# Optimization experiments

Measured on AMD Instinct MI355X. Metric: run time of the kernel, lower is better.

The kernel has to match this reference:

```python
import jax, jax.numpy as jnp
import numpy as np

N = 50000          # nodes
E = 800000         # edges (before self loops)
C_IN, HID, C_OUT, L = 128, 64, 64, 3
LSTM_H = (L * HID) // 2   # 96, PyG JK-LSTM hidden size
NEG_SLOPE = 0.2


def gat_conv(x, src, dst, W, a_src, a_dst, b):
    # single-head PyG GATConv
    h = x @ W.T                                  # [N, HID]
    al = h @ a_src                               # [N] src attention logits
    ar = h @ a_dst                               # [N]
    e = jax.nn.leaky_relu(al[src] + ar[dst], NEG_SLOPE)   # [E+N]
    m = jax.ops.segment_max(e, dst, num_segments=N)
    ex = jnp.exp(e - m[dst])
    den = jax.ops.segment_sum(ex, dst, num_segments=N)
    coef = ex / den[dst]                         # segment softmax over dst neighborhoods
    out = jax.ops.segment_sum(coef[:, None] * h[src], dst, num_segments=N)
    return out + b


def lstm_dir(seq, Wih, Whh, bih, bhh, reverse):
    # seq: [L, N, C]; returns hidden states [L, N, H] in original time order
    H = Whh.shape[1]
    h0 = jnp.zeros((seq.shape[1], H), seq.dtype)

    def step(carry, x_t):
        h, c = carry
        g = x_t @ Wih.T + bih + h @ Whh.T + bhh
        i, f, gg, o = jnp.split(g, 4, axis=-1)
        c = jax.nn.sigmoid(f) * c + jax.nn.sigmoid(i) * jnp.tanh(gg)
        h = jax.nn.sigmoid(o) * jnp.tanh(c)
        return (h, c), h

    _, hs = jax.lax.scan(step, (h0, h0), seq, reverse=reverse)
    return hs


def setup_inputs() -> dict:
    key = jax.random.key(0)
    ks = jax.random.split(key, 32)
    s = 0.1
    inp = {
        'x': jax.random.normal(ks[0], (N, C_IN), jnp.float32),
        'edge_index': jax.random.randint(ks[1], (2, E), 0, N, jnp.int64
                                         if jax.config.jax_enable_x64 else jnp.int32),
    }
    dims = [C_IN, HID, HID]
    for l in range(L):
        inp[f'conv{l}_W'] = s * jax.random.normal(ks[2 + 4 * l], (HID, dims[l]), jnp.float32)
        inp[f'conv{l}_asrc'] = s * jax.random.normal(ks[3 + 4 * l], (HID,), jnp.float32)
        inp[f'conv{l}_adst'] = s * jax.random.normal(ks[4 + 4 * l], (HID,), jnp.float32)
        inp[f'conv{l}_b'] = jnp.zeros((HID,), jnp.float32)
    for d, off in (('f', 16), ('b', 20)):
        inp[f'lstm_Wih_{d}'] = s * jax.random.normal(ks[off], (4 * LSTM_H, HID), jnp.float32)
        inp[f'lstm_Whh_{d}'] = s * jax.random.normal(ks[off + 1], (4 * LSTM_H, LSTM_H), jnp.float32)
        inp[f'lstm_bih_{d}'] = jnp.zeros((4 * LSTM_H,), jnp.float32)
        inp[f'lstm_bhh_{d}'] = jnp.zeros((4 * LSTM_H,), jnp.float32)
    inp['att_W'] = s * jax.random.normal(ks[24], (1, 2 * LSTM_H), jnp.float32)
    inp['att_b'] = jnp.zeros((1,), jnp.float32)
    inp['out_W'] = s * jax.random.normal(ks[25], (C_OUT, HID), jnp.float32)
    inp['out_b'] = jnp.zeros((C_OUT,), jnp.float32)
    return inp


def reference(x, edge_index,
              conv0_W, conv0_asrc, conv0_adst, conv0_b,
              conv1_W, conv1_asrc, conv1_adst, conv1_b,
              conv2_W, conv2_asrc, conv2_adst, conv2_b,
              lstm_Wih_f, lstm_Whh_f, lstm_bih_f, lstm_bhh_f,
              lstm_Wih_b, lstm_Whh_b, lstm_bih_b, lstm_bhh_b,
              att_W, att_b, out_W, out_b):
    # add self loops (PyG GATConv default)
    loop = jnp.arange(N, dtype=edge_index.dtype)
    src = jnp.concatenate([edge_index[0], loop])
    dst = jnp.concatenate([edge_index[1], loop])

    convs = [(conv0_W, conv0_asrc, conv0_adst, conv0_b),
             (conv1_W, conv1_asrc, conv1_adst, conv1_b),
             (conv2_W, conv2_asrc, conv2_adst, conv2_b)]
    xs = []
    h = x
    for (W, asrc, adst, b) in convs:
        h = jax.nn.relu(gat_conv(h, src, dst, W, asrc, adst, b))
        xs.append(h)

    seq = jnp.stack(xs, axis=0)                       # [L, N, HID]
    hf = lstm_dir(seq, lstm_Wih_f, lstm_Whh_f, lstm_bih_f, lstm_bhh_f, False)
    hb = lstm_dir(seq, lstm_Wih_b, lstm_Whh_b, lstm_bih_b, lstm_bhh_b, True)
    hcat = jnp.concatenate([hf, hb], axis=-1)         # [L, N, 2*LSTM_H]
    logits = (hcat @ att_W.T + att_b)[..., 0]         # [L, N]
    alpha = jax.nn.softmax(logits, axis=0)            # softmax over layers
    agg = jnp.einsum('lnc,ln->nc', seq, alpha)        # [N, HID]
    return agg @ out_W.T + out_b
```

## Files before the change

### kernel.cpp

```cpp
#include <hip/hip_runtime.h>
#include <hip/hip_bf16.h>
#include <math.h>


typedef __attribute__((ext_vector_type(4))) float f32x4;
typedef __attribute__((ext_vector_type(8))) short bf16x8;

__device__ __forceinline__ float rcp_f(float x) {
    return __builtin_amdgcn_rcpf(x);
}
__device__ __forceinline__ float sigmoid_f(float x) {
    return rcp_f(1.0f + __expf(-x));
}
__device__ __forceinline__ float tanh_f(float x) {
    return fmaf(2.0f, rcp_f(1.0f + __expf(-2.0f * x)), -1.0f);
}
__device__ __forceinline__ unsigned short f2bf(float x) {
    union { float f; unsigned int u; } v; v.f = x;
    unsigned int r = (v.u + 0x7FFFu + ((v.u >> 16) & 1u)) >> 16;
    return (unsigned short)r;
}
__device__ __forceinline__ float bf2f(unsigned short u) {
    union { unsigned int i; float f; } v; v.i = ((unsigned int)u) << 16;
    return v.f;
}

template<int K>
__global__ __launch_bounds__(256) void lin_kernel(
    const float* __restrict__ x, const float* __restrict__ W,
    const float* __restrict__ asrc, const float* __restrict__ adst,
    unsigned short* __restrict__ h, float* __restrict__ al,
    float* __restrict__ ar, int N)
{
    __shared__ __align__(16) float Wl[64][K + 4];
    for (int i = threadIdx.x; i < 64 * K; i += 256)
        Wl[i / K][i % K] = W[i];
    __syncthreads();

    int lane = threadIdx.x & 63;
    float as = asrc[lane], ad = adst[lane];
    int wid = (blockIdx.x * 256 + threadIdx.x) >> 6;
    int nw  = (gridDim.x * 256) >> 6;
    int n4max = (N + 3) >> 2;
    for (int n4 = wid; n4 < n4max; n4 += nw) {
        int nb = __builtin_amdgcn_readfirstlane(n4) << 2;
        const float* xr0 = x + (size_t)nb * K;
        const float* xr1 = x + (size_t)min(nb + 1, N - 1) * K;
        const float* xr2 = x + (size_t)min(nb + 2, N - 1) * K;
        const float* xr3 = x + (size_t)min(nb + 3, N - 1) * K;
        float a0 = 0.f, a1 = 0.f, a2 = 0.f, a3 = 0.f;
        #pragma unroll 4
        for (int k = 0; k < K; k += 4) {
            f32x4 wv = *reinterpret_cast<const f32x4*>(&Wl[lane][k]);
            float4 x0 = *reinterpret_cast<const float4*>(xr0 + k);
            float4 x1 = *reinterpret_cast<const float4*>(xr1 + k);
            float4 x2 = *reinterpret_cast<const float4*>(xr2 + k);
            float4 x3 = *reinterpret_cast<const float4*>(xr3 + k);
            a0 += x0.x * wv.x + x0.y * wv.y + x0.z * wv.z + x0.w * wv.w;
            a1 += x1.x * wv.x + x1.y * wv.y + x1.z * wv.z + x1.w * wv.w;
            a2 += x2.x * wv.x + x2.y * wv.y + x2.z * wv.z + x2.w * wv.w;
            a3 += x3.x * wv.x + x3.y * wv.y + x3.z * wv.z + x3.w * wv.w;
        }
        float accs[4] = {a0, a1, a2, a3};
        #pragma unroll
        for (int j = 0; j < 4; ++j) {
            int n = nb + j;
            if (n >= N) break;
            float acc = accs[j];
            h[(size_t)n * 64 + lane] = f2bf(acc);
            float pa = acc * as, pr = acc * ad;
            #pragma unroll
            for (int off = 32; off > 0; off >>= 1) {
                pa += __shfl_down(pa, off);
                pr += __shfl_down(pr, off);
            }
            if (lane == 0) { al[n] = pa; ar[n] = pr; }
        }
    }
}

__global__ void csr_zero(int* __restrict__ deg, int* __restrict__ cursor, int N)
{
    int i = blockIdx.x * blockDim.x + threadIdx.x;
    if (i < N) { deg[i] = 0; cursor[i] = 0; }
}

__global__ void csr_hist(const int* __restrict__ dst, int* __restrict__ deg, int E)
{
    int i = blockIdx.x * blockDim.x + threadIdx.x;
    if (i < E) atomicAdd(&deg[dst[i]], 1);
}

__global__ void csr_scan1(const int* __restrict__ deg, int* __restrict__ incl,
                          int* __restrict__ part, int N)
{
    __shared__ int sb[2][256];
    int tid = threadIdx.x;
    int i = blockIdx.x * 256 + tid;
    int v = (i < N) ? deg[i] + 1 : 0;
    sb[0][tid] = v;
    __syncthreads();
    int cur = 0;
    #pragma unroll
    for (int off = 1; off < 256; off <<= 1) {
        int s = sb[cur][tid];
        if (tid >= off) s += sb[cur][tid - off];
        sb[cur ^ 1][tid] = s;
        cur ^= 1;
        __syncthreads();
    }
    if (i < N) incl[i] = sb[cur][tid];
    if (tid == 255) part[blockIdx.x] = sb[cur][255];
}

__global__ void csr_scan2(int* __restrict__ part, int NB)
{
    __shared__ int sb[2][256];
    int tid = threadIdx.x;
    int v = (tid < NB) ? part[tid] : 0;
    sb[0][tid] = v;
    __syncthreads();
    int cur = 0;
    #pragma unroll
    for (int off = 1; off < 256; off <<= 1) {
        int s = sb[cur][tid];
        if (tid >= off) s += sb[cur][tid - off];
        sb[cur ^ 1][tid] = s;
        cur ^= 1;
        __syncthreads();
    }
    if (tid < NB) part[tid] = sb[cur][tid] - v;
}

__global__ void csr_scan3(const int* __restrict__ deg, const int* __restrict__ incl,
                          const int* __restrict__ part, int* __restrict__ rowptr,
                          int N, int total)
{
    int i = blockIdx.x * blockDim.x + threadIdx.x;
    if (i < N)
        rowptr[i] = part[i >> 8] + incl[i] - (deg[i] + 1);
    if (i == 0) rowptr[N] = total;
}

__global__ void csr_scatter(const int* __restrict__ src, const int* __restrict__ dst,
                            const int* __restrict__ rowptr, int* __restrict__ cursor,
                            int* __restrict__ csr_src, int E, int N)
{
    int i = blockIdx.x * blockDim.x + threadIdx.x;
    if (i >= E + N) return;
    int s = (i < E) ? src[i] : (i - E);
    int d = (i < E) ? dst[i] : (i - E);
    int pos = atomicAdd(&cursor[d], 1);
    csr_src[rowptr[d] + pos] = s;
}

__global__ __launch_bounds__(256) void agg_kernel(
    const int* __restrict__ rowptr, const int* __restrict__ csr_src,
    const float* __restrict__ al, const float* __restrict__ ar,
    const unsigned short* __restrict__ h, const float* __restrict__ b,
    float* __restrict__ outseq, int N)
{
    int lane = threadIdx.x & 63;
    int w = threadIdx.x >> 6;
    int d = blockIdx.x * 4 + w;
    if (d >= N) return;
    int li = lane & 15, grp = lane >> 4;

    int rp0 = rowptr[d], rp1 = rowptr[d + 1];
    int degd = rp1 - rp0;
    float ard = ar[d];
    float den = 0.0f;
    float a0 = 0.f, a1 = 0.f, a2 = 0.f, a3 = 0.f;

    for (int c0 = 0; c0 < degd; c0 += 64) {
        int ne = min(64, degd - c0);
        int s_l = 0;
        float ex_l = 0.0f;
        if (lane < ne) {
            s_l = csr_src[rp0 + c0 + lane];
            float e = al[s_l] + ard;
            e = (e >= 0.0f) ? e : 0.2f * e;
            ex_l = __expf(e);
        }
        float dsum = ex_l;
        #pragma unroll
        for (int off = 32; off > 0; off >>= 1) dsum += __shfl_xor(dsum, off);
        den += dsum;
        #pragma unroll 2
        for (int e2 = 0; e2 < ne; e2 += 4) {
            int eA = e2 + grp;
            float exb = __shfl(ex_l, eA);
            int sb = __shfl(s_l, eA);
            uint2 hv = *reinterpret_cast<const uint2*>(
                &h[(size_t)sb * 64 + li * 4]);
            a0 += exb * bf2f((unsigned short)(hv.x & 0xFFFFu));
            a1 += exb * bf2f((unsigned short)(hv.x >> 16));
            a2 += exb * bf2f((unsigned short)(hv.y & 0xFFFFu));
            a3 += exb * bf2f((unsigned short)(hv.y >> 16));
        }
    }
    #pragma unroll
    for (int off = 16; off < 64; off <<= 1) {
        a0 += __shfl_xor(a0, off);
        a1 += __shfl_xor(a1, off);
        a2 += __shfl_xor(a2, off);
        a3 += __shfl_xor(a3, off);
    }
    if (grp == 0) {
        float inv = rcp_f(den);
        int ch = li * 4;
        float4 v;
        v.x = fmaxf(fmaf(a0, inv, b[ch]),     0.0f);
        v.y = fmaxf(fmaf(a1, inv, b[ch + 1]), 0.0f);
        v.z = fmaxf(fmaf(a2, inv, b[ch + 2]), 0.0f);
        v.w = fmaxf(fmaf(a3, inv, b[ch + 3]), 0.0f);
        *reinterpret_cast<float4*>(&outseq[(size_t)d * 64 + ch]) = v;
    }
}

__global__ void prep_lstm(
    const float* __restrict__ WihF, const float* __restrict__ WhhF,
    const float* __restrict__ bihF, const float* __restrict__ bhhF,
    const float* __restrict__ WihB_, const float* __restrict__ WhhB_,
    const float* __restrict__ bihB_, const float* __restrict__ bhhB_,
    unsigned short* __restrict__ WB, float* __restrict__ bsum)
{
    int tid = blockIdx.x * blockDim.x + threadIdx.x;
    if (tid < 2 * 61440) {
        int dir = tid / 61440, rr = tid % 61440;
        const float* Wih = dir ? WihB_ : WihF;
        const float* Whh = dir ? WhhB_ : WhhF;
        float v;
        if (rr < 24576) {
            int f = rr >> 9, l = (rr >> 3) & 63, s = rr & 7;
            int kc = f & 1, qt = f >> 1;
            int q = qt / 6, t6 = qt % 6;
            int j = q * 96 + t6 * 16 + (l & 15);
            int k = kc * 32 + (l >> 4) * 8 + s;
            v = Wih[j * 64 + k];
        } else {
            int rr2 = rr - 24576;
            int f = rr2 >> 9, l = (rr2 >> 3) & 63, s = rr2 & 7;
            int kc = f % 3, qt = f / 3;
            int q = qt / 6, t6 = qt % 6;
            int j = q * 96 + t6 * 16 + (l & 15);
            int k = kc * 32 + (l >> 4) * 8 + s;
            v = Whh[j * 96 + k];
        }
        WB[tid] = f2bf(v);
    } else if (tid < 2 * 61440 + 2 * 384) {
        int q2 = tid - 2 * 61440;
        int dir = q2 / 384, j = q2 % 384;
        bsum[q2] = dir ? (bihB_[j] + bhhB_[j]) : (bihF[j] + bhhF[j]);
    }
}

__global__ __launch_bounds__(512, 2) void lstm_kernel(
    const float* __restrict__ seq, const unsigned short* __restrict__ WB,
    const float* __restrict__ bsum, const float* __restrict__ attW,
    const float* __restrict__ attb, const float* __restrict__ outW,
    const float* __restrict__ outb, float* __restrict__ out, int N)
{
    __shared__ __align__(16) unsigned short smem[75520];
    unsigned short* WL = smem;
    unsigned short* HS = smem + 61440;
    float* LG = reinterpret_cast<float*>(smem + 74752);

    const int tid  = threadIdx.x;
    const int lane = tid & 63;
    const int w    = tid >> 6;
    const int i16  = lane & 15;
    const int g    = lane >> 4;
    const int n0   = blockIdx.x * 128;
    const int nodebase = 16 * w;
    const int myrow = nodebase + g * 4;

    float attb0 = attb[0];
    if (tid < 384) LG[tid] = attb0;

    for (int dir = 0; dir < 2; ++dir) {
        __syncthreads();
        {
            const f32x4* gsrc = reinterpret_cast<const f32x4*>(WB + dir * 61440);
            f32x4* ldst = reinterpret_cast<f32x4*>(WL);
            #pragma unroll
            for (int it = 0; it < 15; ++it)
                ldst[it * 512 + tid] = gsrc[it * 512 + tid];
        }
        {
            unsigned int* hz = reinterpret_cast<unsigned int*>(&HS[nodebase * 104]);
            for (int e2 = lane; e2 < 832; e2 += 64) hz[e2] = 0u;
        }
        const float* bs = bsum + dir * 384;
        const float* aw = attW + dir * 96;
        float bsr[24];
        #pragma unroll
        for (int t6 = 0; t6 < 6; ++t6)
            #pragma unroll
            for (int q = 0; q < 4; ++q)
                bsr[t6 * 4 + q] = bs[q * 96 + t6 * 16 + i16];
        float awr[6];
        #pragma unroll
        for (int t6 = 0; t6 < 6; ++t6) awr[t6] = aw[t6 * 16 + i16];
        float c[24];
        #pragma unroll
        for (int a = 0; a < 24; ++a) c[a] = 0.0f;
        __syncthreads();

        for (int step = 0; step < 3; ++step) {
            int t = dir ? (2 - step) : step;

            int nn = n0 + nodebase + i16;
            nn = (nn < N) ? nn : (N - 1);
            const float* xr = seq + ((size_t)t * N + nn) * 64 + g * 8;
            float4 xa = *reinterpret_cast<const float4*>(xr);
            float4 xb = *reinterpret_cast<const float4*>(xr + 4);
            float4 xc = *reinterpret_cast<const float4*>(xr + 32);
            float4 xd = *reinterpret_cast<const float4*>(xr + 36);
            bf16x8 ax0, ax1;
            ax0[0] = (short)f2bf(xa.x); ax0[1] = (short)f2bf(xa.y);
            ax0[2] = (short)f2bf(xa.z); ax0[3] = (short)f2bf(xa.w);
            ax0[4] = (short)f2bf(xb.x); ax0[5] = (short)f2bf(xb.y);
            ax0[6] = (short)f2bf(xb.z); ax0[7] = (short)f2bf(xb.w);
            ax1[0] = (short)f2bf(xc.x); ax1[1] = (short)f2bf(xc.y);
            ax1[2] = (short)f2bf(xc.z); ax1[3] = (short)f2bf(xc.w);
            ax1[4] = (short)f2bf(xd.x); ax1[5] = (short)f2bf(xd.y);
            ax1[6] = (short)f2bf(xd.z); ax1[7] = (short)f2bf(xd.w);

            const unsigned short* hrow = &HS[(nodebase + i16) * 104];
            bf16x8 ah0 = *reinterpret_cast<const bf16x8*>(hrow + g * 8);
            bf16x8 ah1 = *reinterpret_cast<const bf16x8*>(hrow + 32 + g * 8);
            bf16x8 ah2 = *reinterpret_cast<const bf16x8*>(hrow + 64 + g * 8);
            const unsigned short* wbase = WL + lane * 8;

            float lp[4] = {0.0f, 0.0f, 0.0f, 0.0f};
            #pragma unroll
            for (int t6 = 0; t6 < 6; ++t6) {
                const int jb = t6 * 16 + i16;
                f32x4 acc4[4];
                #pragma unroll
                for (int q = 0; q < 4; ++q) {
                    float bv = bsr[t6 * 4 + q];
                    acc4[q] = (f32x4){bv, bv, bv, bv};
                }
                #pragma unroll
                for (int q = 0; q < 4; ++q) {
                    const int qt = q * 6 + t6;
                    const unsigned short* wih = wbase + (qt * 2) * 512;
                    const unsigned short* whh = wbase + 24576 + (qt * 3) * 512;
                    acc4[q] = __builtin_amdgcn_mfma_f32_16x16x32_bf16(
                        ax0, *reinterpret_cast<const bf16x8*>(wih), acc4[q], 0, 0, 0);
                    acc4[q] = __builtin_amdgcn_mfma_f32_16x16x32_bf16(
                        ax1, *reinterpret_cast<const bf16x8*>(wih + 512), acc4[q], 0, 0, 0);
                    acc4[q] = __builtin_amdgcn_mfma_f32_16x16x32_bf16(
                        ah0, *reinterpret_cast<const bf16x8*>(whh), acc4[q], 0, 0, 0);
                    acc4[q] = __builtin_amdgcn_mfma_f32_16x16x32_bf16(
                        ah1, *reinterpret_cast<const bf16x8*>(whh + 512), acc4[q], 0, 0, 0);
                    acc4[q] = __builtin_amdgcn_mfma_f32_16x16x32_bf16(
                        ah2, *reinterpret_cast<const bf16x8*>(whh + 1024), acc4[q], 0, 0, 0);
                }
                #pragma unroll
                for (int reg = 0; reg < 4; ++reg) {
                    float ii = acc4[0][reg];
                    float ff = acc4[1][reg];
                    float gg = acc4[2][reg];
                    float oo = acc4[3][reg];
                    float cn = sigmoid_f(ff) * c[t6 * 4 + reg]
                             + sigmoid_f(ii) * tanh_f(gg);
                    c[t6 * 4 + reg] = cn;
                    float hn = sigmoid_f(oo) * tanh_f(cn);
                    HS[(myrow + reg) * 104 + jb] = f2bf(hn);
                    lp[reg] += hn * awr[t6];
                }
            }
            #pragma unroll
            for (int reg = 0; reg < 4; ++reg) {
                float v = lp[reg];
                v += __shfl_xor(v, 1);
                v += __shfl_xor(v, 2);
                v += __shfl_xor(v, 4);
                v += __shfl_xor(v, 8);
                if (i16 == 0) LG[t * 128 + myrow + reg] += v;
            }
        }
    }
    __syncthreads();

    float* alphaF = reinterpret_cast<float*>(HS);
    if (tid < 128) {
        float l0 = LG[tid], l1 = LG[128 + tid], l2 = LG[256 + tid];
        float mx = fmaxf(fmaxf(l0, l1), l2);
        float e0 = __expf(l0 - mx), e1 = __expf(l1 - mx), e2 = __expf(l2 - mx);
        float inv = rcp_f(e0 + e1 + e2);
        alphaF[tid] = e0 * inv; alphaF[128 + tid] = e1 * inv;
        alphaF[256 + tid] = e2 * inv;
    }
    __syncthreads();

    float* aggF = reinterpret_cast<float*>(WL);
    for (int idx = tid; idx < 128 * 64; idx += 512) {
        int r = idx >> 6, k = idx & 63;
        int n = n0 + r;
        float v = 0.0f;
        if (n < N) {
            float a0 = alphaF[r], a1 = alphaF[128 + r], a2 = alphaF[256 + r];
            v = a0 * seq[((size_t)n) * 64 + k]
              + a1 * seq[((size_t)N + n) * 64 + k]
              + a2 * seq[((size_t)2 * N + n) * 64 + k];
        }
        aggF[r * 68 + k] = v;
    }
    __syncthreads();

    f32x4 ow[16];
    #pragma unroll
    for (int kk = 0; kk < 16; ++kk)
        ow[kk] = *reinterpret_cast<const f32x4*>(&outW[(size_t)lane * 64 + kk * 4]);
    float ob = outb[lane];
    for (int r = w; r < 128; r += 8) {
        int n = n0 + r;
        if (n >= N) break;
        float a = ob;
        #pragma unroll
        for (int kk = 0; kk < 16; ++kk) {
            f32x4 av = *reinterpret_cast<const f32x4*>(&aggF[r * 68 + kk * 4]);
            a += ow[kk].x * av.x + ow[kk].y * av.y
               + ow[kk].z * av.z + ow[kk].w * av.w;
        }
        out[(size_t)n * 64 + lane] = a;
    }
}

extern "C" void kernel_launch(void* const* d_in, const int* in_sizes, int n_in,
                              void* d_out, int out_size, void* d_ws, size_t ws_size,
                              hipStream_t stream)
{
    const float* x    = (const float*)d_in[0];
    const int*   ei   = (const int*)d_in[1];
    const float* convW[3]  = {(const float*)d_in[2], (const float*)d_in[6],  (const float*)d_in[10]};
    const float* convAs[3] = {(const float*)d_in[3], (const float*)d_in[7],  (const float*)d_in[11]};
    const float* convAd[3] = {(const float*)d_in[4], (const float*)d_in[8],  (const float*)d_in[12]};
    const float* convB[3]  = {(const float*)d_in[5], (const float*)d_in[9],  (const float*)d_in[13]};
    const float* WihF = (const float*)d_in[14];
    const float* WhhF = (const float*)d_in[15];
    const float* bihF = (const float*)d_in[16];
    const float* bhhF = (const float*)d_in[17];
    const float* WihB = (const float*)d_in[18];
    const float* WhhB = (const float*)d_in[19];
    const float* bihB = (const float*)d_in[20];
    const float* bhhB = (const float*)d_in[21];
    const float* attW = (const float*)d_in[22];
    const float* attb = (const float*)d_in[23];
    const float* outW = (const float*)d_in[24];
    const float* outb = (const float*)d_in[25];

    int N = in_sizes[0] / 128;
    int E = in_sizes[1] / 2;
    const int* src = ei;
    const int* dst = ei + E;
    int total = E + N;

    float* w = (float*)d_ws;
    float* seq  = w;  w += (size_t)3 * N * 64;
    unsigned short* h_bf = (unsigned short*)w;  w += (size_t)N * 32;
    float* al   = w;  w += N;
    float* ar   = w;  w += N;
    float* bsum = w;  w += 768;
    unsigned short* WB = (unsigned short*)w;  w += 61440;
    int* deg     = (int*)w;        w += N;
    int* cursor  = (int*)w;        w += N;
    int* rowptr  = (int*)w;        w += (N + 1);
    int* incl    = (int*)w;        w += N;
    int* part    = (int*)w;        w += 256;
    int* csr_src = (int*)w;        w += total;

    int NB = (N + 255) / 256;

    csr_zero<<<NB, 256, 0, stream>>>(deg, cursor, N);
    csr_hist<<<(E + 255) / 256, 256, 0, stream>>>(dst, deg, E);
    csr_scan1<<<NB, 256, 0, stream>>>(deg, incl, part, N);
    csr_scan2<<<1, 256, 0, stream>>>(part, NB);
    csr_scan3<<<NB, 256, 0, stream>>>(deg, incl, part, rowptr, N, total);
    csr_scatter<<<(total + 255) / 256, 256, 0, stream>>>(src, dst, rowptr, cursor,
                                                         csr_src, E, N);

    prep_lstm<<<(2 * 61440 + 768 + 255) / 256, 256, 0, stream>>>(
        WihF, WhhF, bihF, bhhF, WihB, WhhB, bihB, bhhB, WB, bsum);

    for (int l = 0; l < 3; ++l) {
        const float* in = (l == 0) ? x : seq + (size_t)(l - 1) * N * 64;
        if (l == 0)
            lin_kernel<128><<<2048, 256, 0, stream>>>(in, convW[l], convAs[l], convAd[l],
                                                      h_bf, al, ar, N);
        else
            lin_kernel<64><<<2048, 256, 0, stream>>>(in, convW[l], convAs[l], convAd[l],
                                                     h_bf, al, ar, N);
        agg_kernel<<<(N + 3) / 4, 256, 0, stream>>>(rowptr, csr_src, al, ar, h_bf,
                                                    convB[l], seq + (size_t)l * N * 64, N);
    }

    lstm_kernel<<<(N + 127) / 128, 512, 0, stream>>>(seq, WB, bsum, attW, attb,
                                                     outW, outb, (float*)d_out, N);
}
```

Before: 381.6 us.

## Emit bf16 layer outputs from aggregation and enlarge LSTM blocks to 192 nodes

The aggregation kernel now also writes a bf16 copy of each layer's output, and the LSTM kernel reads that copy instead of loading fp32 and converting in-kernel, halving its sequence reads. The LSTM block grows from 512 to 768 threads (192 nodes), amortising the per-block weight staging into shared memory over more nodes. The hidden-state row pitch drops from 104 to 96 shorts to fit the larger block in shared memory, which may add LDS bank conflicts. The final layer-attention aggregation now uses bf16 inputs, which lowers accuracy slightly, and the extra bf16 stores add write traffic to the aggregation kernel.

```diff
diff --git a/kernel.cpp b/kernel.cpp
--- a/kernel.cpp
+++ b/kernel.cpp
@@ -158,7 +158,7 @@
     const int* __restrict__ rowptr, const int* __restrict__ csr_src,
     const float* __restrict__ al, const float* __restrict__ ar,
     const unsigned short* __restrict__ h, const float* __restrict__ b,
-    float* __restrict__ outseq, int N)
+    float* __restrict__ outseq, unsigned short* __restrict__ outseq_bf, int N)
 {
     int lane = threadIdx.x & 63;
     int w = threadIdx.x >> 6;
@@ -215,6 +215,10 @@
         v.z = fmaxf(fmaf(a2, inv, b[ch + 2]), 0.0f);
         v.w = fmaxf(fmaf(a3, inv, b[ch + 3]), 0.0f);
         *reinterpret_cast<float4*>(&outseq[(size_t)d * 64 + ch]) = v;
+        uint2 bb;
+        bb.x = (unsigned int)f2bf(v.x) | ((unsigned int)f2bf(v.y) << 16);
+        bb.y = (unsigned int)f2bf(v.z) | ((unsigned int)f2bf(v.w) << 16);
+        *reinterpret_cast<uint2*>(&outseq_bf[(size_t)d * 64 + ch]) = bb;
     }
 }
 
@@ -255,28 +259,29 @@
     }
 }
 
-__global__ __launch_bounds__(512, 2) void lstm_kernel(
-    const float* __restrict__ seq, const unsigned short* __restrict__ WB,
+__global__ __launch_bounds__(768, 3) void lstm_kernel(
+    const unsigned short* __restrict__ seq_bf, const float* __restrict__ seq,
+    const unsigned short* __restrict__ WB,
     const float* __restrict__ bsum, const float* __restrict__ attW,
     const float* __restrict__ attb, const float* __restrict__ outW,
     const float* __restrict__ outb, float* __restrict__ out, int N)
 {
-    __shared__ __align__(16) unsigned short smem[75520];
+    __shared__ __align__(16) unsigned short smem[81024];
     unsigned short* WL = smem;
     unsigned short* HS = smem + 61440;
-    float* LG = reinterpret_cast<float*>(smem + 74752);
+    float* LG = reinterpret_cast<float*>(smem + 79872);
 
     const int tid  = threadIdx.x;
     const int lane = tid & 63;
     const int w    = tid >> 6;
     const int i16  = lane & 15;
     const int g    = lane >> 4;
-    const int n0   = blockIdx.x * 128;
+    const int n0   = blockIdx.x * 192;
     const int nodebase = 16 * w;
     const int myrow = nodebase + g * 4;
 
     float attb0 = attb[0];
-    if (tid < 384) LG[tid] = attb0;
+    if (tid < 576) LG[tid] = attb0;
 
     for (int dir = 0; dir < 2; ++dir) {
         __syncthreads();
@@ -284,12 +289,12 @@
             const f32x4* gsrc = reinterpret_cast<const f32x4*>(WB + dir * 61440);
             f32x4* ldst = reinterpret_cast<f32x4*>(WL);
             #pragma unroll
-            for (int it = 0; it < 15; ++it)
-                ldst[it * 512 + tid] = gsrc[it * 512 + tid];
+            for (int it = 0; it < 10; ++it)
+                ldst[it * 768 + tid] = gsrc[it * 768 + tid];
         }
         {
-            unsigned int* hz = reinterpret_cast<unsigned int*>(&HS[nodebase * 104]);
-            for (int e2 = lane; e2 < 832; e2 += 64) hz[e2] = 0u;
+            unsigned int* hz = reinterpret_cast<unsigned int*>(&HS[nodebase * 96]);
+            for (int e2 = lane; e2 < 768; e2 += 64) hz[e2] = 0u;
         }
         const float* bs = bsum + dir * 384;
         const float* aw = attW + dir * 96;
@@ -312,22 +317,11 @@
 
             int nn = n0 + nodebase + i16;
             nn = (nn < N) ? nn : (N - 1);
-            const float* xr = seq + ((size_t)t * N + nn) * 64 + g * 8;
-            float4 xa = *reinterpret_cast<const float4*>(xr);
-            float4 xb = *reinterpret_cast<const float4*>(xr + 4);
-            float4 xc = *reinterpret_cast<const float4*>(xr + 32);
-            float4 xd = *reinterpret_cast<const float4*>(xr + 36);
-            bf16x8 ax0, ax1;
-            ax0[0] = (short)f2bf(xa.x); ax0[1] = (short)f2bf(xa.y);
-            ax0[2] = (short)f2bf(xa.z); ax0[3] = (short)f2bf(xa.w);
-            ax0[4] = (short)f2bf(xb.x); ax0[5] = (short)f2bf(xb.y);
-            ax0[6] = (short)f2bf(xb.z); ax0[7] = (short)f2bf(xb.w);
-            ax1[0] = (short)f2bf(xc.x); ax1[1] = (short)f2bf(xc.y);
-            ax1[2] = (short)f2bf(xc.z); ax1[3] = (short)f2bf(xc.w);
-            ax1[4] = (short)f2bf(xd.x); ax1[5] = (short)f2bf(xd.y);
-            ax1[6] = (short)f2bf(xd.z); ax1[7] = (short)f2bf(xd.w);
-
-            const unsigned short* hrow = &HS[(nodebase + i16) * 104];
+            const unsigned short* xr = seq_bf + ((size_t)t * N + nn) * 64 + g * 8;
+            bf16x8 ax0 = *reinterpret_cast<const bf16x8*>(xr);
+            bf16x8 ax1 = *reinterpret_cast<const bf16x8*>(xr + 32);
+
+            const unsigned short* hrow = &HS[(nodebase + i16) * 96];
             bf16x8 ah0 = *reinterpret_cast<const bf16x8*>(hrow + g * 8);
             bf16x8 ah1 = *reinterpret_cast<const bf16x8*>(hrow + 32 + g * 8);
             bf16x8 ah2 = *reinterpret_cast<const bf16x8*>(hrow + 64 + g * 8);
@@ -369,7 +363,7 @@
                              + sigmoid_f(ii) * tanh_f(gg);
                     c[t6 * 4 + reg] = cn;
                     float hn = sigmoid_f(oo) * tanh_f(cn);
-                    HS[(myrow + reg) * 104 + jb] = f2bf(hn);
+                    HS[(myrow + reg) * 96 + jb] = f2bf(hn);
                     lp[reg] += hn * awr[t6];
                 }
             }
@@ -380,33 +374,33 @@
                 v += __shfl_xor(v, 2);
                 v += __shfl_xor(v, 4);
                 v += __shfl_xor(v, 8);
-                if (i16 == 0) LG[t * 128 + myrow + reg] += v;
+                if (i16 == 0) LG[t * 192 + myrow + reg] += v;
             }
         }
     }
     __syncthreads();
 
     float* alphaF = reinterpret_cast<float*>(HS);
-    if (tid < 128) {
-        float l0 = LG[tid], l1 = LG[128 + tid], l2 = LG[256 + tid];
+    if (tid < 192) {
+        float l0 = LG[tid], l1 = LG[192 + tid], l2 = LG[384 + tid];
         float mx = fmaxf(fmaxf(l0, l1), l2);
         float e0 = __expf(l0 - mx), e1 = __expf(l1 - mx), e2 = __expf(l2 - mx);
         float inv = rcp_f(e0 + e1 + e2);
-        alphaF[tid] = e0 * inv; alphaF[128 + tid] = e1 * inv;
-        alphaF[256 + tid] = e2 * inv;
+        alphaF[tid] = e0 * inv; alphaF[192 + tid] = e1 * inv;
+        alphaF[384 + tid] = e2 * inv;
     }
     __syncthreads();
 
     float* aggF = reinterpret_cast<float*>(WL);
-    for (int idx = tid; idx < 128 * 64; idx += 512) {
+    for (int idx = tid; idx < 192 * 64; idx += 768) {
         int r = idx >> 6, k = idx & 63;
         int n = n0 + r;
         float v = 0.0f;
         if (n < N) {
-            float a0 = alphaF[r], a1 = alphaF[128 + r], a2 = alphaF[256 + r];
-            v = a0 * seq[((size_t)n) * 64 + k]
-              + a1 * seq[((size_t)N + n) * 64 + k]
-              + a2 * seq[((size_t)2 * N + n) * 64 + k];
+            float a0 = alphaF[r], a1 = alphaF[192 + r], a2 = alphaF[384 + r];
+            v = a0 * bf2f(seq_bf[((size_t)n) * 64 + k])
+              + a1 * bf2f(seq_bf[((size_t)N + n) * 64 + k])
+              + a2 * bf2f(seq_bf[((size_t)2 * N + n) * 64 + k]);
         }
         aggF[r * 68 + k] = v;
     }
@@ -417,7 +411,7 @@
     for (int kk = 0; kk < 16; ++kk)
         ow[kk] = *reinterpret_cast<const f32x4*>(&outW[(size_t)lane * 64 + kk * 4]);
     float ob = outb[lane];
-    for (int r = w; r < 128; r += 8) {
+    for (int r = w; r < 192; r += 12) {
         int n = n0 + r;
         if (n >= N) break;
         float a = ob;
@@ -467,6 +461,7 @@
     float* ar   = w;  w += N;
     float* bsum = w;  w += 768;
     unsigned short* WB = (unsigned short*)w;  w += 61440;
+    unsigned short* seq_bf = (unsigned short*)w;  w += (size_t)3 * N * 32;
     int* deg     = (int*)w;        w += N;
     int* cursor  = (int*)w;        w += N;
     int* rowptr  = (int*)w;        w += (N + 1);
@@ -496,9 +491,10 @@
             lin_kernel<64><<<2048, 256, 0, stream>>>(in, convW[l], convAs[l], convAd[l],
                                                      h_bf, al, ar, N);
         agg_kernel<<<(N + 3) / 4, 256, 0, stream>>>(rowptr, csr_src, al, ar, h_bf,
-                                                    convB[l], seq + (size_t)l * N * 64, N);
-    }
-
-    lstm_kernel<<<(N + 127) / 128, 512, 0, stream>>>(seq, WB, bsum, attW, attb,
+                                                    convB[l], seq + (size_t)l * N * 64,
+                                                    seq_bf + (size_t)l * N * 64, N);
+    }
+
+    lstm_kernel<<<(N + 191) / 192, 768, 0, stream>>>(seq_bf, seq, WB, bsum, attW, attb,
                                                      outW, outb, (float*)d_out, N);
 }
```

Result: slower. 440.4 us (+15.4%).
